# Kernel tuning notes

Measured on AMD Instinct MI355X. Metric: run time of the kernel, lower is better.

Reference implementation:

```python
import jax, jax.numpy as jnp
import numpy as np

HEADS = 8
DIM_HEAD = 16          # dim/heads, per default dim_head=None
_DIM = HEADS * DIM_HEAD  # 128
SCALE = DIM_HEAD ** 0.5


def setup_inputs() -> dict:
    key = jax.random.key(0)
    k1, k2, k3 = jax.random.split(key, 3)
    field, batch, dim = 2048, 4, 128
    x = jax.random.normal(k1, (field, batch, dim), dtype=jnp.float32)
    W_qkv = jax.random.normal(k2, (3 * _DIM, dim), dtype=jnp.float32) * (dim ** -0.5)
    W_0 = jax.random.normal(k3, (dim, _DIM), dtype=jnp.float32) * (_DIM ** -0.5)
    b_0 = jnp.zeros((dim,), dtype=jnp.float32)
    return {"x": x, "W_qkv": W_qkv, "W_0": W_0, "b_0": b_0}


def reference(x, W_qkv, W_0, b_0):
    f, b, dim = x.shape
    qkv = x @ W_qkv.T                                  # (f, b, 3*_DIM)
    # reshape (f, b, heads*dim_head) -> (f, b*heads, dim_head), matching torch row-major reshape
    q = qkv[:, :, :_DIM].reshape(f, b * HEADS, DIM_HEAD)
    k = qkv[:, :, _DIM:2 * _DIM].reshape(f, b * HEADS, DIM_HEAD)
    v = qkv[:, :, 2 * _DIM:].reshape(f, b * HEADS, DIM_HEAD)
    # scores over the field axis: (b*heads, f, f)
    scores = jnp.einsum('iqd,jqd->qij', q, k) / SCALE
    attn = jax.nn.softmax(scores, axis=-1)
    out = jnp.einsum('qij,jqd->qid', attn, v)          # (b*heads, f, dim_head)
    out = out.transpose(1, 0, 2)                       # (f, b*heads, dim_head)
    # rearrange 'f (b h) d -> (f b) (h d)'
    out = out.reshape(f, b, HEADS, DIM_HEAD).reshape(f * b, HEADS * DIM_HEAD)
    out = out @ W_0.T + b_0                            # (f*b, dim)
    return out.reshape(f, b, dim)
```

## Files before the change

kernel.cpp:

```cpp
#include <hip/hip_runtime.h>
#include <hip/hip_bf16.h>

#define F_DIM 2048
#define B_DIM 4
#define DIM 128
#define QKV_COLS 384
#define HEADS 8
#define DH 16

#define SHIFT2 14.4269504f
#define QSCALE 0.360673760f

typedef float float4v __attribute__((ext_vector_type(4)));
typedef short short4v __attribute__((ext_vector_type(4)));

static __device__ __forceinline__ unsigned short f2bf(float v) {
    __hip_bfloat16 h = __float2bfloat16(v);
    return __builtin_bit_cast(unsigned short, h);
}

static __device__ __forceinline__ short4v pack_bf16x4(float a, float b, float c, float d) {
    unsigned plo, phi;
    asm("v_cvt_pk_bf16_f32 %0, %1, %2" : "=v"(plo) : "v"(a), "v"(b));
    asm("v_cvt_pk_bf16_f32 %0, %1, %2" : "=v"(phi) : "v"(c), "v"(d));
    uint2 u{plo, phi};
    return __builtin_bit_cast(short4v, u);
}


__global__ __launch_bounds__(384) void qkv_kernel(const float* __restrict__ x,
                                                  const float* __restrict__ Wqkv,
                                                  unsigned short* __restrict__ Qbf,
                                                  unsigned short* __restrict__ Kbf,
                                                  unsigned short* __restrict__ VTt) {
    __shared__ float xs[16 * DIM];
    __shared__ float sA[QKV_COLS * 17];
    const int rbase = blockIdx.x * 16;
    const int fbase = rbase >> 2;
    const int tid = threadIdx.x;
    for (int idx = tid; idx < 16 * DIM; idx += 384)
        xs[idx] = x[(size_t)rbase * DIM + idx];
    __syncthreads();

    const int c = tid;
    const float4* wrow = (const float4*)(Wqkv + (size_t)c * DIM);
    const float4* xs4 = (const float4*)xs;
    float acc[16];
#pragma unroll
    for (int r = 0; r < 16; ++r) acc[r] = 0.f;

    for (int k4 = 0; k4 < DIM / 4; ++k4) {
        float4 wv = wrow[k4];
#pragma unroll
        for (int r = 0; r < 16; ++r) {
            float4 xv = xs4[r * (DIM / 4) + k4];
            acc[r] = fmaf(wv.x, xv.x, acc[r]);
            acc[r] = fmaf(wv.y, xv.y, acc[r]);
            acc[r] = fmaf(wv.z, xv.z, acc[r]);
            acc[r] = fmaf(wv.w, xv.w, acc[r]);
        }
    }
#pragma unroll
    for (int r = 0; r < 16; ++r) sA[c * 17 + r] = acc[r];
    __syncthreads();

    if (tid < 256) {
        const int which = tid >> 7;
        const int u = tid & 127;
        const int ff = u & 3, hh = (u >> 2) & 7, bb = u >> 5;
        const int r = ff * 4 + bb;
        const int cbase = which * 128 + hh * 16;
        const float scale = which ? 1.f : QSCALE;
        unsigned short tmp[16];
#pragma unroll
        for (int d = 0; d < 16; ++d)
            tmp[d] = f2bf(sA[(cbase + d) * 17 + r] * scale);
        unsigned short* dst = (which ? Kbf : Qbf)
            + ((size_t)(bb * 8 + hh) * F_DIM + (fbase + ff)) * DH;
        ((uint4*)dst)[0] = ((const uint4*)tmp)[0];
        ((uint4*)dst)[1] = ((const uint4*)tmp)[1];
    } else {
        const int u = tid - 256;
#pragma unroll
        for (int s = 0; s < 4; ++s) {
            const int ch = u * 4 + s;
            const int dd = ch & 15, hh = (ch >> 4) & 7, bb = ch >> 7;
            const int cc = 256 + hh * 16 + dd;
            unsigned short tmp[4];
#pragma unroll
            for (int ff = 0; ff < 4; ++ff)
                tmp[ff] = f2bf(sA[cc * 17 + ff * 4 + bb]);
            unsigned short* dst = VTt
                + (((size_t)(bb * 8 + hh) * 128 + (fbase >> 4)) * 16 + dd) * 16
                + (fbase & 15);
            *(uint2*)dst = *(const uint2*)tmp;
        }
    }
}

__global__ __launch_bounds__(512, 4) void attn_mfma_kernel(const unsigned short* __restrict__ Qbf,
                                                           const unsigned short* __restrict__ Kbf,
                                                           const unsigned short* __restrict__ VTt,
                                                           float* __restrict__ attn) {
    __shared__ float4v comb[2][3][64][5];

    const int bh = blockIdx.y;
    const int b = bh >> 3, h = bh & 7;
    const int lane = threadIdx.x & 63;
    const int wid = threadIdx.x >> 6;
    const int qg = wid & 1;
    const int ch = wid >> 1;
    const int q0 = blockIdx.x * 128 + qg * 64;
    const int lo = lane & 15, hi = lane >> 4;

    const unsigned short* Qp = Qbf + ((size_t)bh * F_DIM + q0 + lo) * DH + hi * 4;
    const short4v qf0 = *(const short4v*)(Qp);
    const short4v qf1 = *(const short4v*)(Qp + 16 * DH);
    const short4v qf2 = *(const short4v*)(Qp + 32 * DH);
    const short4v qf3 = *(const short4v*)(Qp + 48 * DH);

    const unsigned short* Kp = Kbf + (size_t)bh * F_DIM * DH
                             + (size_t)ch * 512 * DH + (size_t)lo * DH + hi * 4;
    const unsigned short* Vp = VTt + ((size_t)bh * 128 + ch * 32) * 256
                             + lo * 16 + hi * 4;

    float4v acc0 = {0.f, 0.f, 0.f, 0.f};
    float4v acc1 = {0.f, 0.f, 0.f, 0.f};
    float4v acc2 = {0.f, 0.f, 0.f, 0.f};
    float4v acc3 = {0.f, 0.f, 0.f, 0.f};
    float4v la0 = {0.f, 0.f, 0.f, 0.f};
    float4v la1 = {0.f, 0.f, 0.f, 0.f};
    float4v la2 = {0.f, 0.f, 0.f, 0.f};
    float4v la3 = {0.f, 0.f, 0.f, 0.f};
    const float4v cinit = {-SHIFT2, -SHIFT2, -SHIFT2, -SHIFT2};

#pragma unroll 2
    for (int kt = 0; kt < 32; ++kt) {
        const short4v kf = *(const short4v*)(Kp + kt * 256);
        const short4v vf = *(const short4v*)(Vp + kt * 256);

        float4v s0 = __builtin_amdgcn_mfma_f32_16x16x16bf16_1k(kf, qf0, cinit, 0, 0, 0);
        float4v s1 = __builtin_amdgcn_mfma_f32_16x16x16bf16_1k(kf, qf1, cinit, 0, 0, 0);
        float4v s2 = __builtin_amdgcn_mfma_f32_16x16x16bf16_1k(kf, qf2, cinit, 0, 0, 0);
        float4v s3 = __builtin_amdgcn_mfma_f32_16x16x16bf16_1k(kf, qf3, cinit, 0, 0, 0);

        float p00 = __builtin_amdgcn_exp2f(s0[0]), p01 = __builtin_amdgcn_exp2f(s0[1]);
        float p02 = __builtin_amdgcn_exp2f(s0[2]), p03 = __builtin_amdgcn_exp2f(s0[3]);
        float p10 = __builtin_amdgcn_exp2f(s1[0]), p11 = __builtin_amdgcn_exp2f(s1[1]);
        float p12 = __builtin_amdgcn_exp2f(s1[2]), p13 = __builtin_amdgcn_exp2f(s1[3]);
        float p20 = __builtin_amdgcn_exp2f(s2[0]), p21 = __builtin_amdgcn_exp2f(s2[1]);
        float p22 = __builtin_amdgcn_exp2f(s2[2]), p23 = __builtin_amdgcn_exp2f(s2[3]);
        float p30 = __builtin_amdgcn_exp2f(s3[0]), p31 = __builtin_amdgcn_exp2f(s3[1]);
        float p32 = __builtin_amdgcn_exp2f(s3[2]), p33 = __builtin_amdgcn_exp2f(s3[3]);

        la0[0] += p00; la0[1] += p01; la0[2] += p02; la0[3] += p03;
        la1[0] += p10; la1[1] += p11; la1[2] += p12; la1[3] += p13;
        la2[0] += p20; la2[1] += p21; la2[2] += p22; la2[3] += p23;
        la3[0] += p30; la3[1] += p31; la3[2] += p32; la3[3] += p33;

        short4v pa0 = pack_bf16x4(p00, p01, p02, p03);
        short4v pa1 = pack_bf16x4(p10, p11, p12, p13);
        short4v pa2 = pack_bf16x4(p20, p21, p22, p23);
        short4v pa3 = pack_bf16x4(p30, p31, p32, p33);

        acc0 = __builtin_amdgcn_mfma_f32_16x16x16bf16_1k(pa0, vf, acc0, 0, 0, 0);
        acc1 = __builtin_amdgcn_mfma_f32_16x16x16bf16_1k(pa1, vf, acc1, 0, 0, 0);
        acc2 = __builtin_amdgcn_mfma_f32_16x16x16bf16_1k(pa2, vf, acc2, 0, 0, 0);
        acc3 = __builtin_amdgcn_mfma_f32_16x16x16bf16_1k(pa3, vf, acc3, 0, 0, 0);
    }

    float l0 = (la0[0] + la0[1]) + (la0[2] + la0[3]);
    float l1 = (la1[0] + la1[1]) + (la1[2] + la1[3]);
    float l2 = (la2[0] + la2[1]) + (la2[2] + la2[3]);
    float l3 = (la3[0] + la3[1]) + (la3[2] + la3[3]);

    if (ch) {
        float4v* pw = comb[qg][ch - 1][lane];
        pw[0] = acc0; pw[1] = acc1; pw[2] = acc2; pw[3] = acc3;
        float4v lv = {l0, l1, l2, l3};
        pw[4] = lv;
    }
    __syncthreads();
    if (!ch) {
#pragma unroll
        for (int part = 0; part < 3; ++part) {
            const float4v* pr = comb[qg][part][lane];
            acc0 += pr[0]; acc1 += pr[1]; acc2 += pr[2]; acc3 += pr[3];
            float4v tl = pr[4];
            l0 += tl[0]; l1 += tl[1]; l2 += tl[2]; l3 += tl[3];
        }

#define STORE_FRAG(ACC, L, FR)                                                  \
        {                                                                       \
            float l = L;                                                        \
            l += __shfl_xor(l, 16);                                             \
            l += __shfl_xor(l, 32);                                             \
            float inv = 1.f / l;                          \
            _Pragma("unroll")                                                   \
            for (int r = 0; r < 4; ++r) {                                       \
                int q = hi * 4 + r;                                             \
                float invq = __shfl(inv, q);                                    \
                int f = q0 + (FR) * 16 + q;                                     \
                attn[((size_t)f * B_DIM + b) * DIM + h * DH + lo] = ACC[r] * invq; \
            }                                                                   \
        }
        STORE_FRAG(acc0, l0, 0)
        STORE_FRAG(acc1, l1, 1)
        STORE_FRAG(acc2, l2, 2)
        STORE_FRAG(acc3, l3, 3)
#undef STORE_FRAG
    }
}

__global__ __launch_bounds__(256) void proj_kernel(const float* __restrict__ attn,
                                                   const float* __restrict__ W0,
                                                   const float* __restrict__ b0,
                                                   float* __restrict__ out) {
    __shared__ float as_[8 * DIM];
    const int rbase = blockIdx.x * 8;
    const int tid = threadIdx.x;
    for (int idx = tid; idx < 8 * DIM; idx += 256)
        as_[idx] = attn[(size_t)rbase * DIM + idx];
    __syncthreads();

    const int c = tid & 127;
    const int rh = tid >> 7;
    const float4* wrow = (const float4*)(W0 + (size_t)c * DIM);
    const float4* as4 = (const float4*)(as_ + rh * 4 * DIM);
    float acc[4] = {0.f, 0.f, 0.f, 0.f};

    for (int k4 = 0; k4 < DIM / 4; ++k4) {
        float4 wv = wrow[k4];
#pragma unroll
        for (int r = 0; r < 4; ++r) {
            float4 xv = as4[r * (DIM / 4) + k4];
            acc[r] = fmaf(wv.x, xv.x, acc[r]);
            acc[r] = fmaf(wv.y, xv.y, acc[r]);
            acc[r] = fmaf(wv.z, xv.z, acc[r]);
            acc[r] = fmaf(wv.w, xv.w, acc[r]);
        }
    }
    const float bias = b0[c];
#pragma unroll
    for (int r = 0; r < 4; ++r)
        out[(size_t)(rbase + rh * 4 + r) * DIM + c] = acc[r] + bias;
}

extern "C" void kernel_launch(void* const* d_in, const int* in_sizes, int n_in,
                              void* d_out, int out_size, void* d_ws, size_t ws_size,
                              hipStream_t stream) {
    const float* x    = (const float*)d_in[0];
    const float* Wqkv = (const float*)d_in[1];
    const float* W0   = (const float*)d_in[2];
    const float* b0   = (const float*)d_in[3];
    float* out = (float*)d_out;

    char* ws = (char*)d_ws;
    float* attn          = (float*)(ws);
    unsigned short* Qbf  = (unsigned short*)(ws + (4u << 20));
    unsigned short* Kbf  = (unsigned short*)(ws + (6u << 20));
    unsigned short* VTt  = (unsigned short*)(ws + (8u << 20));

    qkv_kernel<<<512, 384, 0, stream>>>(x, Wqkv, Qbf, Kbf, VTt);
    attn_mfma_kernel<<<dim3(16, 32), 512, 0, stream>>>(Qbf, Kbf, VTt, attn);
    proj_kernel<<<1024, 256, 0, stream>>>(attn, W0, b0, out);
}
```

Baseline: 73.03 us.

## Replace scalar FP32 QKV projection with bf16 MFMA using split-x hi/lo precision

New measurement: 68.46 us. 1.07x faster.

```diff
diff --git a/kernel.cpp b/kernel.cpp
--- a/kernel.cpp
+++ b/kernel.cpp
@@ -18,6 +18,10 @@
     __hip_bfloat16 h = __float2bfloat16(v);
     return __builtin_bit_cast(unsigned short, h);
 }
+static __device__ __forceinline__ float bf2f(unsigned short u) {
+    unsigned int w = ((unsigned int)u) << 16;
+    return __builtin_bit_cast(float, w);
+}
 
 static __device__ __forceinline__ short4v pack_bf16x4(float a, float b, float c, float d) {
     unsigned plo, phi;
@@ -28,72 +32,99 @@
 }
 
 
-__global__ __launch_bounds__(384) void qkv_kernel(const float* __restrict__ x,
-                                                  const float* __restrict__ Wqkv,
-                                                  unsigned short* __restrict__ Qbf,
-                                                  unsigned short* __restrict__ Kbf,
-                                                  unsigned short* __restrict__ VTt) {
-    __shared__ float xs[16 * DIM];
-    __shared__ float sA[QKV_COLS * 17];
-    const int rbase = blockIdx.x * 16;
-    const int fbase = rbase >> 2;
-    const int tid = threadIdx.x;
-    for (int idx = tid; idx < 16 * DIM; idx += 384)
-        xs[idx] = x[(size_t)rbase * DIM + idx];
-    __syncthreads();
-
-    const int c = tid;
-    const float4* wrow = (const float4*)(Wqkv + (size_t)c * DIM);
-    const float4* xs4 = (const float4*)xs;
-    float acc[16];
-#pragma unroll
-    for (int r = 0; r < 16; ++r) acc[r] = 0.f;
-
-    for (int k4 = 0; k4 < DIM / 4; ++k4) {
-        float4 wv = wrow[k4];
-#pragma unroll
-        for (int r = 0; r < 16; ++r) {
-            float4 xv = xs4[r * (DIM / 4) + k4];
-            acc[r] = fmaf(wv.x, xv.x, acc[r]);
-            acc[r] = fmaf(wv.y, xv.y, acc[r]);
-            acc[r] = fmaf(wv.z, xv.z, acc[r]);
-            acc[r] = fmaf(wv.w, xv.w, acc[r]);
-        }
-    }
-#pragma unroll
-    for (int r = 0; r < 16; ++r) sA[c * 17 + r] = acc[r];
-    __syncthreads();
-
-    if (tid < 256) {
-        const int which = tid >> 7;
-        const int u = tid & 127;
-        const int ff = u & 3, hh = (u >> 2) & 7, bb = u >> 5;
-        const int r = ff * 4 + bb;
-        const int cbase = which * 128 + hh * 16;
-        const float scale = which ? 1.f : QSCALE;
-        unsigned short tmp[16];
-#pragma unroll
-        for (int d = 0; d < 16; ++d)
-            tmp[d] = f2bf(sA[(cbase + d) * 17 + r] * scale);
-        unsigned short* dst = (which ? Kbf : Qbf)
-            + ((size_t)(bb * 8 + hh) * F_DIM + (fbase + ff)) * DH;
-        ((uint4*)dst)[0] = ((const uint4*)tmp)[0];
-        ((uint4*)dst)[1] = ((const uint4*)tmp)[1];
+__global__ __launch_bounds__(256) void convert_kernel(const float* __restrict__ x,
+                                                      const float* __restrict__ Wqkv,
+                                                      unsigned short* __restrict__ xhi,
+                                                      unsigned short* __restrict__ xlo,
+                                                      unsigned short* __restrict__ Wbf) {
+    const int tid = blockIdx.x * 256 + threadIdx.x;
+    if (blockIdx.x < 512) {
+        const size_t base = (size_t)tid * 8;
+        float v[8];
+        *(float4*)(v)     = *(const float4*)(x + base);
+        *(float4*)(v + 4) = *(const float4*)(x + base + 4);
+        unsigned short h[8], l[8];
+#pragma unroll
+        for (int j = 0; j < 8; ++j) {
+            h[j] = f2bf(v[j]);
+            l[j] = f2bf(v[j] - bf2f(h[j]));
+        }
+        *(uint4*)(xhi + base) = *(const uint4*)h;
+        *(uint4*)(xlo + base) = *(const uint4*)l;
     } else {
-        const int u = tid - 256;
-#pragma unroll
-        for (int s = 0; s < 4; ++s) {
-            const int ch = u * 4 + s;
-            const int dd = ch & 15, hh = (ch >> 4) & 7, bb = ch >> 7;
-            const int cc = 256 + hh * 16 + dd;
-            unsigned short tmp[4];
-#pragma unroll
-            for (int ff = 0; ff < 4; ++ff)
-                tmp[ff] = f2bf(sA[cc * 17 + ff * 4 + bb]);
+        const int t = tid - 512 * 256;
+        const size_t base = (size_t)t * 8;
+        if (base < (size_t)QKV_COLS * DIM) {
+            const int c = (int)(base >> 7);
+            const float scale = (c < 128) ? QSCALE : 1.f;
+            float v[8];
+            *(float4*)(v)     = *(const float4*)(Wqkv + base);
+            *(float4*)(v + 4) = *(const float4*)(Wqkv + base + 4);
+            unsigned short h[8];
+#pragma unroll
+            for (int j = 0; j < 8; ++j) h[j] = f2bf(v[j] * scale);
+            *(uint4*)(Wbf + base) = *(const uint4*)h;
+        }
+    }
+}
+
+__global__ __launch_bounds__(256) void qkv_mfma_kernel(const unsigned short* __restrict__ xhi,
+                                                       const unsigned short* __restrict__ xlo,
+                                                       const unsigned short* __restrict__ Wbf,
+                                                       unsigned short* __restrict__ Qbf,
+                                                       unsigned short* __restrict__ Kbf,
+                                                       unsigned short* __restrict__ VTt) {
+    const int lane = threadIdx.x & 63;
+    const int wid = threadIdx.x >> 6;
+    const int rbase = blockIdx.x * 64 + wid * 16;
+    const int ctbase = blockIdx.y * 6;
+    const int lo = lane & 15, hi = lane >> 4;
+
+    const unsigned short* xph = xhi + (size_t)(rbase + lo) * DIM + hi * 4;
+    const unsigned short* xpl = xlo + (size_t)(rbase + lo) * DIM + hi * 4;
+    short4v xfh[8], xfl[8];
+#pragma unroll
+    for (int kb = 0; kb < 8; ++kb) {
+        xfh[kb] = *(const short4v*)(xph + kb * 16);
+        xfl[kb] = *(const short4v*)(xpl + kb * 16);
+    }
+
+    float4v d[6];
+#pragma unroll
+    for (int j = 0; j < 6; ++j) d[j] = (float4v){0.f, 0.f, 0.f, 0.f};
+
+    const unsigned short* wp = Wbf + (size_t)(ctbase * 16 + lo) * DIM + hi * 4;
+#pragma unroll
+    for (int j = 0; j < 6; ++j) {
+#pragma unroll
+        for (int kb = 0; kb < 8; ++kb) {
+            short4v wf = *(const short4v*)(wp + (size_t)j * 16 * DIM + kb * 16);
+            d[j] = __builtin_amdgcn_mfma_f32_16x16x16bf16_1k(wf, xfh[kb], d[j], 0, 0, 0);
+            d[j] = __builtin_amdgcn_mfma_f32_16x16x16bf16_1k(wf, xfl[kb], d[j], 0, 0, 0);
+        }
+    }
+
+    const int i = rbase + lo;
+    const int f = i >> 2, bb = i & 3;
+#pragma unroll
+    for (int j = 0; j < 6; ++j) {
+        const int ct = ctbase + j;
+        short4v pv = pack_bf16x4(d[j][0], d[j][1], d[j][2], d[j][3]);
+        if (ct < 8) {
+            unsigned short* dst = Qbf + ((size_t)(bb * 8 + ct) * F_DIM + f) * DH + hi * 4;
+            *(uint2*)dst = __builtin_bit_cast(uint2, pv);
+        } else if (ct < 16) {
+            unsigned short* dst = Kbf + ((size_t)(bb * 8 + (ct - 8)) * F_DIM + f) * DH + hi * 4;
+            *(uint2*)dst = __builtin_bit_cast(uint2, pv);
+        } else {
+            const int hh = ct - 16;
             unsigned short* dst = VTt
-                + (((size_t)(bb * 8 + hh) * 128 + (fbase >> 4)) * 16 + dd) * 16
-                + (fbase & 15);
-            *(uint2*)dst = *(const uint2*)tmp;
+                + (((size_t)(bb * 8 + hh) * 128 + (f >> 4)) * 16) * 16 + (f & 15);
+#pragma unroll
+            for (int r = 0; r < 4; ++r) {
+                const int dd = hi * 4 + r;
+                dst[(size_t)dd * 16] = (unsigned short)pv[r];
+            }
         }
     }
 }
@@ -260,8 +291,12 @@
     unsigned short* Qbf  = (unsigned short*)(ws + (4u << 20));
     unsigned short* Kbf  = (unsigned short*)(ws + (6u << 20));
     unsigned short* VTt  = (unsigned short*)(ws + (8u << 20));
-
-    qkv_kernel<<<512, 384, 0, stream>>>(x, Wqkv, Qbf, Kbf, VTt);
+    unsigned short* xhi  = (unsigned short*)(ws + (10u << 20));
+    unsigned short* xlo  = (unsigned short*)(ws + (12u << 20));
+    unsigned short* Wbf  = (unsigned short*)(ws + (14u << 20));
+
+    convert_kernel<<<536, 256, 0, stream>>>(x, Wqkv, xhi, xlo, Wbf);
+    qkv_mfma_kernel<<<dim3(128, 4), 256, 0, stream>>>(xhi, xlo, Wbf, Qbf, Kbf, VTt);
     attn_mfma_kernel<<<dim3(16, 32), 512, 0, stream>>>(Qbf, Kbf, VTt, attn);
     proj_kernel<<<1024, 256, 0, stream>>>(attn, W0, b0, out);
 }
```
